# Optimization experiments

Hardware: AMD Instinct MI355X
Metric: run time of the kernel (lower is better)

The kernel has to match this reference:

```python
import jax, jax.numpy as jnp
import numpy as np

DIM = 1024
NUM_HEADS = 16
HEAD_DIM = DIM // NUM_HEADS
SCALE = HEAD_DIM ** -0.5


def setup_inputs() -> dict:
    key = jax.random.key(0)
    k_x, k_qkv, k_pw, k_pb = jax.random.split(key, 4)
    B, N, C = 1, 4096, 3 * DIM
    x = jax.random.normal(k_x, (B, N, C), dtype=jnp.float32)
    # torch nn.Linear stores weight as [out, in]; y = x @ W.T + b
    W_qkv = jax.random.normal(k_qkv, (3 * DIM, 3 * DIM), dtype=jnp.float32) * (3 * DIM) ** -0.5
    W_proj = jax.random.normal(k_pw, (DIM, DIM), dtype=jnp.float32) * DIM ** -0.5
    b_proj = jax.random.normal(k_pb, (DIM,), dtype=jnp.float32) * 0.01
    return {"x": x, "W_qkv": W_qkv, "W_proj": W_proj, "b_proj": b_proj}


def reference(x, W_qkv, W_proj, b_proj):
    B, N, C = x.shape  # C == 3*DIM
    qkv = x @ W_qkv.T  # [B, N, 3*DIM]
    qkv = qkv.reshape(B, N, 3, NUM_HEADS, HEAD_DIM).transpose(2, 0, 3, 1, 4)
    q, k, v = qkv[0], qkv[1], qkv[2]  # each [B, H, N, hd]
    attn = jnp.einsum('bhnd,bhmd->bhnm', q, k) * SCALE
    attn = jax.nn.softmax(attn, axis=-1)
    out = jnp.einsum('bhnm,bhmd->bhnd', attn, v)  # [B, H, N, hd]
    out = out.transpose(0, 2, 1, 3).reshape(B, N, DIM)
    return out @ W_proj.T + b_proj
```

## Files before the change

kernel.cpp:

```cpp
#include <hip/hip_runtime.h>
#include <hip/hip_fp16.h>

#define SEQ     4096
#define NHEADS  16
#define HDIM    64
#define DIMSZ   1024
#define ATT_SCALE 0.125f

static constexpr size_t QSZ = (size_t)NHEADS * SEQ * HDIM;

typedef __attribute__((ext_vector_type(8))) short short8;
typedef __attribute__((ext_vector_type(4))) short s16x4;
typedef __attribute__((ext_vector_type(8))) unsigned short ushort8;
typedef __attribute__((ext_vector_type(4))) float f32x4;
#define MFMA_F16(a, b, c) __builtin_amdgcn_mfma_f32_16x16x32_f16((a), (b), (c), 0, 0, 0)

__device__ __forceinline__ unsigned short f2hu(float x) {
    __half h = __float2half(x);
    return *reinterpret_cast<unsigned short*>(&h);
}
__device__ __forceinline__ float hu2f(unsigned short u) {
    __half h = *reinterpret_cast<__half*>(&u);
    return __half2float(h);
}
__device__ __forceinline__ void split8h(float4 f0, float4 f1, ushort8& h, ushort8& l) {
    const float v[8] = {f0.x, f0.y, f0.z, f0.w, f1.x, f1.y, f1.z, f1.w};
    #pragma unroll
    for (int i = 0; i < 8; ++i) {
        const unsigned short hi = f2hu(v[i]);
        h[i] = hi;
        l[i] = f2hu(v[i] - hu2f(hi));
    }
}

typedef __attribute__((address_space(1))) const unsigned int g_u32;
typedef __attribute__((address_space(3))) unsigned int lds_u32;
__device__ __forceinline__ void async16(unsigned short* lds, const unsigned short* g) {
    __builtin_amdgcn_global_load_lds((g_u32*)g, (lds_u32*)lds, 16, 0, 0);
}

__global__ void prep_split(const float* __restrict__ x, unsigned short* __restrict__ xh,
                           unsigned short* __restrict__ xl, int nx,
                           const float* __restrict__ w0, unsigned short* __restrict__ w0h,
                           int n0,
                           const float* __restrict__ w1, unsigned short* __restrict__ w1h,
                           int n1)
{
    const int stride = gridDim.x * blockDim.x;
    const int tid = blockIdx.x * blockDim.x + threadIdx.x;
    for (int i = tid; i < (nx >> 2); i += stride) {
        float4 v = ((const float4*)x)[i];
        ushort4 h, l;
        h.x = f2hu(v.x); l.x = f2hu(v.x - hu2f(h.x));
        h.y = f2hu(v.y); l.y = f2hu(v.y - hu2f(h.y));
        h.z = f2hu(v.z); l.z = f2hu(v.z - hu2f(h.z));
        h.w = f2hu(v.w); l.w = f2hu(v.w - hu2f(h.w));
        ((ushort4*)xh)[i] = h; ((ushort4*)xl)[i] = l;
    }
    for (int i = tid; i < (n0 >> 2); i += stride) {
        float4 v = ((const float4*)w0)[i];
        ushort4 h;
        h.x = f2hu(v.x); h.y = f2hu(v.y); h.z = f2hu(v.z); h.w = f2hu(v.w);
        ((ushort4*)w0h)[i] = h;
    }
    for (int i = tid; i < (n1 >> 2); i += stride) {
        float4 v = ((const float4*)w1)[i];
        ushort4 h;
        h.x = f2hu(v.x); h.y = f2hu(v.y); h.z = f2hu(v.z); h.w = f2hu(v.w);
        ((ushort4*)w1h)[i] = h;
    }
}

__global__ __launch_bounds__(512, 2)
void qkv_gemm_8ph(const unsigned short* __restrict__ AHg,
                  const unsigned short* __restrict__ ALg,
                  const unsigned short* __restrict__ BHg,
                  unsigned short* __restrict__ QH, unsigned short* __restrict__ QL,
                  unsigned short* __restrict__ KH, unsigned short* __restrict__ VT)
{
    constexpr int K3 = 3072;
    constexpr int NT = K3 / 32;
    __shared__ __align__(16) unsigned short ring[3 * 24576];

    const int t  = threadIdx.x;
    const int wv = t >> 6;
    const int ln = t & 63;
    const int lx = ln & 15;
    const int q4 = ln >> 4;
    const int wr = wv >> 2;
    const int wc = wv & 3;

    const int bid = blockIdx.x;
    const int swz = (bid & 7) * 32 + (bid >> 3);
    const int m0 = (swz >> 4) * 256;
    const int n0 = (swz & 15) * 192;

    const int srow = t >> 2;
    const int sg8  = (((t & 3) ^ ((t >> 3) & 3)) << 3);

    auto stage3a = [&](int tt, int b) {
        const int kk = tt << 5;
        unsigned short* Lb = &ring[b * 24576 + wv * 512];
        const size_t ga = (size_t)(m0 + srow) * K3 + kk + sg8;
        async16(Lb,               AHg + ga);
        async16(Lb + 4096,        AHg + ga + (size_t)128 * K3);
        async16(Lb + 8192,        ALg + ga);
    };
    auto stage3b = [&](int tt, int b) {
        const int kk = tt << 5;
        unsigned short* Lb = &ring[b * 24576 + wv * 512];
        const size_t ga = (size_t)(m0 + srow) * K3 + kk + sg8;
        const size_t gb = (size_t)(n0 + srow) * K3 + kk + sg8;
        async16(Lb + 12288,       ALg + ga + (size_t)128 * K3);
        async16(Lb + 16384,       BHg + gb);
        async16(Lb + 20480,       BHg + gb + (size_t)128 * K3);
    };

    f32x4 acc[8][3];
    #pragma unroll
    for (int mf = 0; mf < 8; ++mf)
        #pragma unroll
        for (int nf = 0; nf < 3; ++nf)
            acc[mf][nf] = (f32x4){0.f, 0.f, 0.f, 0.f};

    stage3a(0, 0); stage3b(0, 0);
    stage3a(1, 1); stage3b(1, 1);
    asm volatile("s_waitcnt vmcnt(6)" ::: "memory");
    __builtin_amdgcn_s_barrier();

    const int aswz8 = ((q4 ^ ((lx >> 1) & 3)) << 3);
    const int arow0 = (wr * 128 + lx) * 32 + aswz8;
    const int brow0 = (wc * 48  + lx) * 32 + aswz8;

    int c = 0;
    for (int kt = 0; kt < NT; ++kt) {
        const unsigned short* AHp = &ring[c * 24576];
        const unsigned short* ALp = AHp + 8192;
        const unsigned short* Bp  = AHp + 16384;
        int c2 = c + 2; if (c2 >= 3) c2 -= 3;
        const bool pf = (kt + 2 < NT);

        short8 bfr[3];
        #pragma unroll
        for (int ph = 0; ph < 4; ++ph) {
            if (ph == 0) {
                #pragma unroll
                for (int nf = 0; nf < 3; ++nf)
                    bfr[nf] = *(const short8*)&Bp[brow0 + nf * 512];
            }
            short8 ahf[2], alf[2];
            #pragma unroll
            for (int i = 0; i < 2; ++i) {
                const int mo = arow0 + (ph * 2 + i) * 512;
                ahf[i] = *(const short8*)&AHp[mo];
                alf[i] = *(const short8*)&ALp[mo];
            }
            if (ph == 0 && pf) stage3a(kt + 2, c2);
            if (ph == 1 && pf) stage3b(kt + 2, c2);
            __builtin_amdgcn_s_barrier();
            __builtin_amdgcn_s_setprio(1);
            #pragma unroll
            for (int nf = 0; nf < 3; ++nf)
                #pragma unroll
                for (int i = 0; i < 2; ++i) {
                    acc[ph * 2 + i][nf] = MFMA_F16(ahf[i], bfr[nf], acc[ph * 2 + i][nf]);
                    acc[ph * 2 + i][nf] = MFMA_F16(alf[i], bfr[nf], acc[ph * 2 + i][nf]);
                }
            __builtin_amdgcn_s_setprio(0);
            if (ph == 3) {
                if (pf) asm volatile("s_waitcnt vmcnt(6)" ::: "memory");
                else    asm volatile("s_waitcnt vmcnt(0)" ::: "memory");
            }
            __builtin_amdgcn_s_barrier();
        }
        ++c; if (c == 3) c = 0;
    }

    #pragma unroll
    for (int nf = 0; nf < 3; ++nf) {
        const int colb = n0 + wc * 48 + nf * 16;
        const int part = colb >> 10;
        const int head = (colb >> 6) & 15;
        const int d0   = (colb & 63) + lx;
        if (part == 0) {
            #pragma unroll
            for (int mf = 0; mf < 8; ++mf) {
                const int row0 = m0 + wr * 128 + mf * 16 + q4 * 4;
                #pragma unroll
                for (int r = 0; r < 4; ++r) {
                    const float v = acc[mf][nf][r] * ATT_SCALE;
                    const unsigned short h = f2hu(v);
                    const size_t idx = ((size_t)head * SEQ + row0 + r) * HDIM + d0;
                    QH[idx] = h;
                    QL[idx] = f2hu(v - hu2f(h));
                }
            }
        } else if (part == 1) {
            #pragma unroll
            for (int mf = 0; mf < 8; ++mf) {
                const int row0 = m0 + wr * 128 + mf * 16 + q4 * 4;
                #pragma unroll
                for (int r = 0; r < 4; ++r) {
                    const size_t idx = ((size_t)head * SEQ + row0 + r) * HDIM + d0;
                    KH[idx] = f2hu(acc[mf][nf][r]);
                }
            }
        } else {
            unsigned short* base = VT + ((size_t)head * HDIM + d0) * SEQ;
            #pragma unroll
            for (int mf = 0; mf < 8; ++mf) {
                const int row0 = m0 + wr * 128 + mf * 16 + q4 * 4;
                ushort4 o;
                o.x = f2hu(acc[mf][nf][0]); o.y = f2hu(acc[mf][nf][1]);
                o.z = f2hu(acc[mf][nf][2]); o.w = f2hu(acc[mf][nf][3]);
                *(ushort4*)(base + row0) = o;
            }
        }
    }
}

template <int MODE, bool ASPLIT>
__global__ __launch_bounds__(256, 3)
void mfma_gemm_abt(const float* __restrict__ A,
                   const unsigned short* __restrict__ AHg,
                   const unsigned short* __restrict__ ALg,
                   const unsigned short* __restrict__ BHg,
                   const float* __restrict__ bias, float* __restrict__ C,
                   unsigned short* __restrict__ QH, unsigned short* __restrict__ QL,
                   unsigned short* __restrict__ KH, unsigned short* __restrict__ VT,
                   int M, int N, int K)
{
    constexpr int LDP = ASPLIT ? 32 : 40;
    __shared__ unsigned short AHs[128 * LDP];
    __shared__ unsigned short ALs[128 * LDP];
    __shared__ unsigned short BHs[128 * LDP];

    const int t  = threadIdx.x;
    const int wv = t >> 6;
    const int ln = t & 63;
    const int lx = ln & 15;
    const int q4 = ln >> 4;
    const int m0 = blockIdx.y * 128;
    const int n0 = blockIdx.x * 128;

    f32x4 acc[2][8];
    #pragma unroll
    for (int mf = 0; mf < 2; ++mf)
        #pragma unroll
        for (int nf = 0; nf < 8; ++nf)
            acc[mf][nf] = (f32x4){0.f, 0.f, 0.f, 0.f};

    for (int k0 = 0; k0 < K; k0 += 32) {
        if constexpr (ASPLIT) {
            const int rowc = ln >> 2;
            const int c8   = (ln & 3) << 3;
            #pragma unroll
            for (int rep = 0; rep < 2; ++rep) {
                const int chunk = rep * 4 + wv;
                const int r = chunk * 16 + rowc;
                const size_t goff = (size_t)(m0 + r) * K + k0 + c8;
                const size_t boff = (size_t)(n0 + r) * K + k0 + c8;
                async16(&AHs[chunk * 16 * LDP], AHg + goff);
                async16(&ALs[chunk * 16 * LDP], ALg + goff);
                async16(&BHs[chunk * 16 * LDP], BHg + boff);
            }
        } else {
            #pragma unroll
            for (int rep = 0; rep < 2; ++rep) {
                const int task = rep * 256 + t;
                const int r  = task >> 2;
                const int sg = (task & 3) << 3;
                {
                    const float* p = A + (size_t)(m0 + r) * K + k0 + sg;
                    float4 f0 = *(const float4*)p;
                    float4 f1 = *(const float4*)(p + 4);
                    ushort8 h, l; split8h(f0, f1, h, l);
                    *(ushort8*)&AHs[r * LDP + sg] = h;
                    *(ushort8*)&ALs[r * LDP + sg] = l;
                }
                {
                    const size_t off = (size_t)(n0 + r) * K + k0 + sg;
                    *(ushort8*)&BHs[r * LDP + sg] = *(const ushort8*)(BHg + off);
                }
            }
        }
        __syncthreads();

        short8 ah[2], al[2];
        #pragma unroll
        for (int mf = 0; mf < 2; ++mf) {
            const int row = wv * 32 + mf * 16 + lx;
            ah[mf] = *(const short8*)&AHs[row * LDP + q4 * 8];
            al[mf] = *(const short8*)&ALs[row * LDP + q4 * 8];
        }
        #pragma unroll
        for (int nf = 0; nf < 8; ++nf) {
            const short8 bh = *(const short8*)&BHs[(nf * 16 + lx) * LDP + q4 * 8];
            #pragma unroll
            for (int mf = 0; mf < 2; ++mf) {
                acc[mf][nf] = MFMA_F16(ah[mf], bh, acc[mf][nf]);
                acc[mf][nf] = MFMA_F16(al[mf], bh, acc[mf][nf]);
            }
        }
        __syncthreads();
    }

    if constexpr (MODE == 0) {
        #pragma unroll
        for (int nf = 0; nf < 8; ++nf) {
            const int col = n0 + nf * 16 + lx;
            const float bv = bias[col];
            #pragma unroll
            for (int mf = 0; mf < 2; ++mf) {
                const int row0 = m0 + wv * 32 + mf * 16 + q4 * 4;
                #pragma unroll
                for (int r = 0; r < 4; ++r)
                    C[(size_t)(row0 + r) * N + col] = acc[mf][nf][r] + bv;
            }
        }
    } else {
        const int part = n0 >> 10;
        #pragma unroll
        for (int nf = 0; nf < 8; ++nf) {
            const int colb = n0 + nf * 16;
            const int head = (colb >> 6) & 15;
            const int d0   = (colb & 63) + lx;
            if (part == 0) {
                #pragma unroll
                for (int mf = 0; mf < 2; ++mf) {
                    const int row0 = m0 + wv * 32 + mf * 16 + q4 * 4;
                    #pragma unroll
                    for (int r = 0; r < 4; ++r) {
                        const float v = acc[mf][nf][r] * ATT_SCALE;
                        const unsigned short h = f2hu(v);
                        const size_t idx = ((size_t)head * SEQ + row0 + r) * HDIM + d0;
                        QH[idx] = h;
                        QL[idx] = f2hu(v - hu2f(h));
                    }
                }
            } else if (part == 1) {
                #pragma unroll
                for (int mf = 0; mf < 2; ++mf) {
                    const int row0 = m0 + wv * 32 + mf * 16 + q4 * 4;
                    #pragma unroll
                    for (int r = 0; r < 4; ++r) {
                        const size_t idx = ((size_t)head * SEQ + row0 + r) * HDIM + d0;
                        KH[idx] = f2hu(acc[mf][nf][r]);
                    }
                }
            } else {
                unsigned short* base = VT + ((size_t)head * HDIM + d0) * SEQ;
                #pragma unroll
                for (int mf = 0; mf < 2; ++mf) {
                    const int row0 = m0 + wv * 32 + mf * 16 + q4 * 4;
                    ushort4 o;
                    o.x = f2hu(acc[mf][nf][0]); o.y = f2hu(acc[mf][nf][1]);
                    o.z = f2hu(acc[mf][nf][2]); o.w = f2hu(acc[mf][nf][3]);
                    *(ushort4*)(base + row0) = o;
                }
            }
        }
    }
}

__global__ __launch_bounds__(256, 2)
void attn_mfma(const unsigned short* __restrict__ QHg,
               const unsigned short* __restrict__ QLg,
               const unsigned short* __restrict__ KHg,
               const unsigned short* __restrict__ VTg,
               unsigned short* __restrict__ AttnH,
               unsigned short* __restrict__ AttnL)
{
    __shared__ __align__(16) char shraw[65536];
    unsigned short* KA = (unsigned short*)shraw;
    unsigned short* VA = (unsigned short*)(shraw + 16384);
    unsigned short* KB = (unsigned short*)(shraw + 32768);
    unsigned short* VB = (unsigned short*)(shraw + 49152);
    float* obuf = (float*)shraw;
    float* lbuf = (float*)(shraw + 34816);

    const int t  = threadIdx.x;
    const int wv = t >> 6;
    const int ln = t & 63;
    const int q4 = ln >> 4;
    const int lx = ln & 15;
    const int qb   = blockIdx.x;
    const int head = blockIdx.y;

    const unsigned short* Kh = KHg + (size_t)head * SEQ * HDIM;
    const unsigned short* Vg = VTg + (size_t)head * HDIM * SEQ;

    short8 qh[4][2], ql[4][2];
    #pragma unroll
    for (int qt = 0; qt < 4; ++qt)
        #pragma unroll
        for (int s = 0; s < 2; ++s) {
            const size_t off = ((size_t)head * SEQ + (size_t)qb * 64 + qt * 16 + lx) * HDIM
                             + s * 32 + q4 * 8;
            qh[qt][s] = *(const short8*)(QHg + off);
            ql[qt][s] = *(const short8*)(QLg + off);
        }

    f32x4 o_acc[4][4];
    float l_part[4] = {0.f, 0.f, 0.f, 0.f};
    #pragma unroll
    for (int dt = 0; dt < 4; ++dt)
        #pragma unroll
        for (int qt = 0; qt < 4; ++qt)
            o_acc[dt][qt] = (f32x4){0.f, 0.f, 0.f, 0.f};

    const int rK8 = t >> 3;
    const int gck = ((t & 7) ^ (rK8 & 7)) << 3;
    const int rV4 = t >> 4;
    const int gcv = ((t & 15) ^ (rV4 & 7)) << 3;

    auto issue_tile = [&](int kbase, unsigned short* KX, unsigned short* VX) {
        #pragma unroll
        for (int c = 0; c < 4; ++c) {
            async16(KX + (c * 32 + wv * 8) * 64,
                    Kh + (size_t)(kbase + c * 32 + rK8) * HDIM + gck);
            async16(VX + (c * 16 + wv * 4) * 128,
                    Vg + (size_t)(c * 16 + rV4) * SEQ + kbase + gcv);
        }
    };

    auto compute_tile = [&](const unsigned short* KX, const unsigned short* VX) {
        short8 phi[4];
        #pragma unroll
        for (int st = 0; st < 2; ++st) {
            const int kr = st * 64 + wv * 16 + lx;
            short8 kfh[2];
            #pragma unroll
            for (int s = 0; s < 2; ++s)
                kfh[s] = *(const short8*)&KX[kr * 64 + (((s * 4 + q4) ^ (kr & 7)) << 3)];
            #pragma unroll
            for (int qt = 0; qt < 4; ++qt) {
                f32x4 sa = (f32x4){0.f, 0.f, 0.f, 0.f};
                __builtin_amdgcn_s_setprio(1);
                #pragma unroll
                for (int s = 0; s < 2; ++s) {
                    sa = MFMA_F16(kfh[s], qh[qt][s], sa);
                    sa = MFMA_F16(kfh[s], ql[qt][s], sa);
                }
                __builtin_amdgcn_s_setprio(0);
                #pragma unroll
                for (int r = 0; r < 4; ++r) {
                    const float e = __expf(sa[r]);
                    l_part[qt] += e;
                    phi[qt][st * 4 + r] = (short)f2hu(e);
                }
            }
        }
        const int colb = wv * 32 + q4 * 8;
        const int sl0  = colb >> 4;
        const int sub  = (colb & 15) >> 1;
        #pragma unroll
        for (int dt = 0; dt < 4; ++dt) {
            const int vr = dt * 16 + lx;
            const s16x4 v0 = *(const s16x4*)&VX[vr * 128 + (((sl0    ) ^ (vr & 7)) << 3) + sub];
            const s16x4 v1 = *(const s16x4*)&VX[vr * 128 + (((sl0 + 8) ^ (vr & 7)) << 3) + sub];
            short8 vf;
            #pragma unroll
            for (int i = 0; i < 4; ++i) { vf[i] = v0[i]; vf[i + 4] = v1[i]; }
            __builtin_amdgcn_s_setprio(1);
            #pragma unroll
            for (int qt = 0; qt < 4; ++qt)
                o_acc[dt][qt] = MFMA_F16(vf, phi[qt], o_acc[dt][qt]);
            __builtin_amdgcn_s_setprio(0);
        }
    };

    issue_tile(0, KA, VA);
    __syncthreads();

    for (int i = 0; i < SEQ / 256; ++i) {
        const int mt = 2 * i;
        if (mt + 1 < SEQ / 128) issue_tile((mt + 1) * 128, KB, VB);
        compute_tile(KA, VA);
        __syncthreads();
        if (mt + 2 < SEQ / 128) issue_tile((mt + 2) * 128, KA, VA);
        compute_tile(KB, VB);
        __syncthreads();
    }

    float lw[4];
    #pragma unroll
    for (int qt = 0; qt < 4; ++qt) {
        float l = l_part[qt];
        l += __shfl_xor(l, 16);
        l += __shfl_xor(l, 32);
        lw[qt] = l;
    }
    if (q4 == 0) {
        #pragma unroll
        for (int qt = 0; qt < 4; ++qt)
            lbuf[wv * 64 + qt * 16 + lx] = lw[qt];
    }
    #pragma unroll
    for (int p = 0; p < 2; ++p) {
        #pragma unroll
        for (int dd = 0; dd < 2; ++dd) {
            const int dt = p * 2 + dd;
            #pragma unroll
            for (int qt = 0; qt < 4; ++qt)
                #pragma unroll
                for (int r = 0; r < 4; ++r)
                    obuf[wv * 2176 + (dd * 16 + q4 * 4 + r) * 68 + qt * 16 + lx]
                        = o_acc[dt][qt][r];
        }
        __syncthreads();
        {
            const int q  = t >> 2;
            const int dg = (t & 3) << 3;
            const float linv = 1.f / (lbuf[q] + lbuf[64 + q] + lbuf[128 + q] + lbuf[192 + q]);
            ushort8 ho, lo;
            #pragma unroll
            for (int j = 0; j < 8; ++j) {
                const int dloc = dg + j;
                const float s = obuf[dloc * 68 + q] + obuf[2176 + dloc * 68 + q]
                              + obuf[4352 + dloc * 68 + q] + obuf[6528 + dloc * 68 + q];
                const float v = s * linv;
                const unsigned short h = f2hu(v);
                ho[j] = (short)h;
                lo[j] = (short)f2hu(v - hu2f(h));
            }
            const size_t ob = (size_t)(qb * 64 + q) * DIMSZ + head * HDIM + p * 32 + dg;
            *(ushort8*)(AttnH + ob) = ho;
            *(ushort8*)(AttnL + ob) = lo;
        }
        __syncthreads();
    }
}

extern "C" void kernel_launch(void* const* d_in, const int* in_sizes, int n_in,
                              void* d_out, int out_size, void* d_ws,
                              size_t ws_size, hipStream_t stream)
{
    const float* x     = (const float*)d_in[0];
    const float* Wqkv  = (const float*)d_in[1];
    const float* Wproj = (const float*)d_in[2];
    const float* bproj = (const float*)d_in[3];
    float* out = (float*)d_out;

    const size_t NWQ = (size_t)3072 * 3072;
    const size_t NWP = (size_t)1024 * 1024;
    const size_t NX  = (size_t)4096 * 3072;

    unsigned short* ub = (unsigned short*)d_ws;
    unsigned short* AttnH = ub;
    unsigned short* AttnL = ub + QSZ;
    unsigned short* QHg = ub + 2 * QSZ;
    unsigned short* QLg = ub + 3 * QSZ;
    unsigned short* KHg = ub + 4 * QSZ;
    unsigned short* VTg = ub + 5 * QSZ;
    unsigned short* WQH = ub + 6 * QSZ;
    unsigned short* WPH = WQH + NWQ;
    unsigned short* XH  = WPH + NWP;
    unsigned short* XL  = XH + NX;
    const bool xsplit = ws_size >= 121634816ull;

    prep_split<<<2048, 256, 0, stream>>>(
        xsplit ? x : nullptr, XH, XL, xsplit ? (int)NX : 0,
        Wqkv, WQH, (int)NWQ, Wproj, WPH, (int)NWP);

    if (xsplit) {
        qkv_gemm_8ph<<<256, 512, 0, stream>>>(
            XH, XL, WQH, QHg, QLg, KHg, VTg);
    } else {
        dim3 g1(3 * DIMSZ / 128, SEQ / 128);
        mfma_gemm_abt<1, false><<<g1, 256, 0, stream>>>(
            x, nullptr, nullptr, WQH, nullptr, nullptr,
            QHg, QLg, KHg, VTg, SEQ, 3 * DIMSZ, 3 * DIMSZ);
    }

    dim3 g2(SEQ / 64, NHEADS);
    attn_mfma<<<g2, 256, 0, stream>>>(QHg, QLg, KHg, VTg, AttnH, AttnL);

    dim3 g3(DIMSZ / 128, SEQ / 128);
    mfma_gemm_abt<0, true><<<g3, 256, 0, stream>>>(
        nullptr, AttnH, AttnL, WPH, bproj, out,
        nullptr, nullptr, nullptr, nullptr, SEQ, DIMSZ, DIMSZ);
}
```

Baseline: 417.7 us.

## Add triple-buffered async-copy projection GEMM and cut per-phase barriers in QKV GEMM

Replaces the generic projection GEMM launch with a dedicated 512-thread kernel. It uses a three-stage shared-memory ring filled by async 16-byte copies, swizzled LDS layout, block-index swizzling and split-fp16 MFMA. Separately, the QKV GEMM drops two barriers per phase and keeps only one barrier per K-tile after the vmcnt wait, which reduces synchronisation stalls. Removing those barriers depends on the ring distance alone to prevent overwriting a buffer other waves are still reading.

```diff
diff --git a/kernel.cpp b/kernel.cpp
--- a/kernel.cpp
+++ b/kernel.cpp
@@ -157,7 +157,6 @@
             }
             if (ph == 0 && pf) stage3a(kt + 2, c2);
             if (ph == 1 && pf) stage3b(kt + 2, c2);
-            __builtin_amdgcn_s_barrier();
             __builtin_amdgcn_s_setprio(1);
             #pragma unroll
             for (int nf = 0; nf < 3; ++nf)
@@ -170,8 +169,8 @@
             if (ph == 3) {
                 if (pf) asm volatile("s_waitcnt vmcnt(6)" ::: "memory");
                 else    asm volatile("s_waitcnt vmcnt(0)" ::: "memory");
-            }
-            __builtin_amdgcn_s_barrier();
+                __builtin_amdgcn_s_barrier();
+            }
         }
         ++c; if (c == 3) c = 0;
     }
@@ -215,6 +214,113 @@
                 o.z = f2hu(acc[mf][nf][2]); o.w = f2hu(acc[mf][nf][3]);
                 *(ushort4*)(base + row0) = o;
             }
+        }
+    }
+}
+
+__global__ __launch_bounds__(512, 2)
+void proj_gemm_r3(const unsigned short* __restrict__ AHg,
+                  const unsigned short* __restrict__ ALg,
+                  const unsigned short* __restrict__ BHg,
+                  const float* __restrict__ bias, float* __restrict__ C)
+{
+    constexpr int K1 = 1024;
+    constexpr int NT = K1 / 32;
+    __shared__ __align__(16) unsigned short ring[3 * 12288];
+
+    const int t  = threadIdx.x;
+    const int wv = t >> 6;
+    const int ln = t & 63;
+    const int lx = ln & 15;
+    const int q4 = ln >> 4;
+    const int wr = wv >> 2;
+    const int wc = wv & 3;
+
+    const int bid = blockIdx.x;
+    const int swz = (bid & 7) * 32 + (bid >> 3);
+    const int m0 = (swz >> 3) * 128;
+    const int n0 = (swz & 7) * 128;
+
+    const int srow = t >> 2;
+    const int sg8  = (((t & 3) ^ ((t >> 3) & 3)) << 3);
+
+    auto stage2a = [&](int tt, int b) {
+        const int kk = tt << 5;
+        unsigned short* Lb = &ring[b * 12288 + wv * 512];
+        const size_t ga = (size_t)(m0 + srow) * K1 + kk + sg8;
+        async16(Lb,               AHg + ga);
+        async16(Lb + 4096,        ALg + ga);
+    };
+    auto stage1b = [&](int tt, int b) {
+        const int kk = tt << 5;
+        unsigned short* Lb = &ring[b * 12288 + wv * 512];
+        const size_t gb = (size_t)(n0 + srow) * K1 + kk + sg8;
+        async16(Lb + 8192,        BHg + gb);
+    };
+
+    f32x4 acc[4][2];
+    #pragma unroll
+    for (int mf = 0; mf < 4; ++mf)
+        #pragma unroll
+        for (int nf = 0; nf < 2; ++nf)
+            acc[mf][nf] = (f32x4){0.f, 0.f, 0.f, 0.f};
+
+    stage2a(0, 0); stage1b(0, 0);
+    stage2a(1, 1); stage1b(1, 1);
+    asm volatile("s_waitcnt vmcnt(3)" ::: "memory");
+    __builtin_amdgcn_s_barrier();
+
+    const int aswz8 = ((q4 ^ ((lx >> 1) & 3)) << 3);
+    const int arow0 = (wr * 64 + lx) * 32 + aswz8;
+    const int brow0 = (wc * 32 + lx) * 32 + aswz8;
+
+    int c = 0;
+    for (int kt = 0; kt < NT; ++kt) {
+        const unsigned short* AHp = &ring[c * 12288];
+        const unsigned short* ALp = AHp + 4096;
+        const unsigned short* Bp  = AHp + 8192;
+        int c2 = c + 2; if (c2 >= 3) c2 -= 3;
+        const bool pf = (kt + 2 < NT);
+
+        short8 bfr[2];
+        #pragma unroll
+        for (int ph = 0; ph < 4; ++ph) {
+            if (ph == 0) {
+                #pragma unroll
+                for (int nf = 0; nf < 2; ++nf)
+                    bfr[nf] = *(const short8*)&Bp[brow0 + nf * 512];
+            }
+            const int mo = arow0 + ph * 512;
+            const short8 ahf = *(const short8*)&AHp[mo];
+            const short8 alf = *(const short8*)&ALp[mo];
+            if (ph == 0 && pf) stage2a(kt + 2, c2);
+            if (ph == 1 && pf) stage1b(kt + 2, c2);
+            __builtin_amdgcn_s_setprio(1);
+            #pragma unroll
+            for (int nf = 0; nf < 2; ++nf) {
+                acc[ph][nf] = MFMA_F16(ahf, bfr[nf], acc[ph][nf]);
+                acc[ph][nf] = MFMA_F16(alf, bfr[nf], acc[ph][nf]);
+            }
+            __builtin_amdgcn_s_setprio(0);
+            if (ph == 3) {
+                if (pf) asm volatile("s_waitcnt vmcnt(3)" ::: "memory");
+                else    asm volatile("s_waitcnt vmcnt(0)" ::: "memory");
+                __builtin_amdgcn_s_barrier();
+            }
+        }
+        ++c; if (c == 3) c = 0;
+    }
+
+    #pragma unroll
+    for (int nf = 0; nf < 2; ++nf) {
+        const int col = n0 + wc * 32 + nf * 16 + lx;
+        const float bv = bias[col];
+        #pragma unroll
+        for (int mf = 0; mf < 4; ++mf) {
+            const int row0 = m0 + wr * 64 + mf * 16 + q4 * 4;
+            #pragma unroll
+            for (int r = 0; r < 4; ++r)
+                C[(size_t)(row0 + r) * DIMSZ + col] = acc[mf][nf][r] + bv;
         }
     }
 }
@@ -576,8 +682,5 @@
     dim3 g2(SEQ / 64, NHEADS);
     attn_mfma<<<g2, 256, 0, stream>>>(QHg, QLg, KHg, VTg, AttnH, AttnL);
 
-    dim3 g3(DIMSZ / 128, SEQ / 128);
-    mfma_gemm_abt<0, true><<<g3, 256, 0, stream>>>(
-        nullptr, AttnH, AttnL, WPH, bproj, out,
-        nullptr, nullptr, nullptr, nullptr, SEQ, DIMSZ, DIMSZ);
-}
+    proj_gemm_r3<<<256, 512, 0, stream>>>(AttnH, AttnL, WPH, bproj, out);
+}
```

Result: faster. 390.5 us (-6.5%).
